# Optimization experiments

Hardware: AMD Instinct MI355X
Metric: run time of the kernel (lower is better)

The kernel has to match this reference:

```python
import jax, jax.numpy as jnp
import numpy as np
from math import sqrt

D_MODEL = 1024
HEADS = 16
D_K = D_MODEL // HEADS
NEG = -1e9


def setup_inputs() -> dict:
    key = jax.random.key(0)
    ks = jax.random.split(key, 8)
    bs, s, d = 2, 2048, D_MODEL
    inp = {
        "k": jax.random.normal(ks[0], (bs, s, d), jnp.float32),
        "v": jax.random.normal(ks[1], (bs, s, d), jnp.float32),
        "q": jax.random.normal(ks[2], (bs, s, d), jnp.float32),
        "mask": jax.random.randint(ks[3], (bs, s, 1), 0, 2).astype(jnp.int64),
        # torch nn.Linear weights: y = x @ W.T, W is [out, in]
        "Wq": jax.random.normal(ks[4], (d, d), jnp.float32) / sqrt(d),
        "Wk": jax.random.normal(ks[5], (d, d), jnp.float32) / sqrt(d),
        "Wv": jax.random.normal(ks[6], (d, d), jnp.float32) / sqrt(d),
        "Wo": jax.random.normal(ks[7], (d, d), jnp.float32) / sqrt(d),
    }
    return inp


def reference(k, v, q, mask, Wq, Wk, Wv, Wo):
    bs, s_k, d = k.shape
    s_q = q.shape[1]
    h, d_k = HEADS, D_K
    # linear projections (no bias), then split heads -> [bs, h, s, d_k]
    kh = (k @ Wk.T).reshape(bs, s_k, h, d_k).transpose(0, 2, 1, 3)
    vh = (v @ Wv.T).reshape(bs, s_k, h, d_k).transpose(0, 2, 1, 3)
    qh = (q @ Wq.T).reshape(bs, s_q, h, d_k).transpose(0, 2, 1, 3)
    # scaled dot-product scores [bs, h, s_q, s_k]
    scores = jnp.einsum("bhqd,bhkd->bhqk", qh, kh) / sqrt(d_k)
    # mask [bs, s_k, 1] -> [bs, 1, 1, s_k], masked positions get -1e9
    m = mask[:, None].transpose(0, 1, 3, 2)  # [bs,1,1,s_k]
    scores = jnp.where(m == 0, NEG, scores)
    probs = jax.nn.softmax(scores, axis=-1)  # dropout is identity (eval)
    attn = jnp.einsum("bhqk,bhkd->bhqd", probs, vh)
    attn_concat = attn.transpose(0, 2, 1, 3).reshape(bs, s_q, d)
    return attn_concat @ Wo.T
```

## Files before the change

### kernel.cpp

```cpp
#include <hip/hip_runtime.h>

typedef __bf16 bf16x8 __attribute__((ext_vector_type(8)));
typedef float f32x4 __attribute__((ext_vector_type(4)));

#define BS 2
#define SEQ 2048
#define DM 1024
#define NH 16
#define DKH 64
#define GM 4096
#define GN 1024
#define GK 1024
#define NEGV (-1e9f)

#define OFF_XQ 0u
#define OFF_XK 4194304u
#define OFF_XV 8388608u
#define OFF_WQ 12582912u
#define OFF_WK 13631488u
#define OFF_WV 14680064u
#define OFF_WO 15728640u
#define OFF_QH 16777216u
#define OFF_KC 20971520u
#define OFF_VT 25165824u
#define OFF_AT OFF_XQ

#if __has_builtin(__builtin_amdgcn_exp2f)
#define EXP2(x) __builtin_amdgcn_exp2f(x)
#else
static __device__ __forceinline__ float EXP2(float x) {
    float r;
    asm volatile("v_exp_f32 %0, %1" : "=v"(r) : "v"(x));
    return r;
}
#endif

__device__ __forceinline__ unsigned cvt_pk(float lo, float hi) {
    unsigned r;
    asm volatile("v_cvt_pk_bf16_f32 %0, %1, %2" : "=v"(r) : "v"(lo), "v"(hi));
    return r;
}

__device__ __forceinline__ unsigned short f2b(float f) {
    unsigned u = __builtin_bit_cast(unsigned, f);
    u += 0x7fffu + ((u >> 16) & 1u);
    return (unsigned short)(u >> 16);
}

typedef const __attribute__((address_space(1))) unsigned int* gas_t;
typedef __attribute__((address_space(3))) unsigned int* las_t;

__device__ __forceinline__ void gload_lds16(const ushort* g, ushort* l) {
    __builtin_amdgcn_global_load_lds((gas_t)(const void*)g, (las_t)(void*)l, 16, 0, 0);
}

#define BARRIER() __builtin_amdgcn_s_barrier()
#define VMCNT(n) asm volatile("s_waitcnt vmcnt(" #n ")" ::: "memory")

__global__ __launch_bounds__(256)
void cvt_kernel(const float* __restrict__ q, const float* __restrict__ k,
                const float* __restrict__ v, const float* __restrict__ wq,
                const float* __restrict__ wk, const float* __restrict__ wv,
                const float* __restrict__ wo, ushort* __restrict__ ws)
{
    const float* src; unsigned n; unsigned dst;
    switch (blockIdx.y) {
        case 0: src = q;  n = 4194304u; dst = OFF_XQ; break;
        case 1: src = k;  n = 4194304u; dst = OFF_XK; break;
        case 2: src = v;  n = 4194304u; dst = OFF_XV; break;
        case 3: src = wq; n = 1048576u; dst = OFF_WQ; break;
        case 4: src = wk; n = 1048576u; dst = OFF_WK; break;
        case 5: src = wv; n = 1048576u; dst = OFF_WV; break;
        default: src = wo; n = 1048576u; dst = OFF_WO; break;
    }
    unsigned i = (blockIdx.x * 256u + threadIdx.x) * 4u;
    if (i >= n) return;
    float4 f = *(const float4*)(src + i);
    ushort4 o;
    o.x = f2b(f.x); o.y = f2b(f.y); o.z = f2b(f.z); o.w = f2b(f.w);
    *(ushort4*)(ws + dst + i) = o;
}

__global__ __launch_bounds__(256)
void scan_kernel(const int* __restrict__ mask, int* __restrict__ cpos, int* __restrict__ mbuf)
{
    const int b = blockIdx.x;
    const int* mp = mask + (size_t)b * SEQ;
    const int tid = threadIdx.x;
    const int lane = tid & 63, w = tid >> 6;
    int v[8];
    int cnt = 0;
#pragma unroll
    for (int j = 0; j < 8; ++j) { v[j] = mp[tid * 8 + j]; cnt += (v[j] != 0); }
    int inc = cnt;
#pragma unroll
    for (int d = 1; d < 64; d <<= 1) {
        int t = __shfl_up(inc, d);
        if (lane >= d) inc += t;
    }
    __shared__ int wsum[4];
    if (lane == 63) wsum[w] = inc;
    __syncthreads();
    int base = inc - cnt;
    for (int i = 0; i < w; ++i) base += wsum[i];
    int c = base;
    int* ob = cpos + (size_t)b * SEQ;
#pragma unroll
    for (int j = 0; j < 8; ++j) {
        ob[tid * 8 + j] = (v[j] != 0) ? c : -1;
        c += (v[j] != 0);
    }
    if (tid == 255) mbuf[b] = base + cnt;
}

__global__ __launch_bounds__(512)
void gemm256(const ushort* __restrict__ Abase, const ushort* __restrict__ Bbase,
             ushort* __restrict__ wsbase, const int* __restrict__ cpos)
{
    __shared__ __align__(16) ushort lA[2][2][8192];
    __shared__ __align__(16) ushort lB[2][2][8192];

    const unsigned z = blockIdx.z;
    const ushort* A  = Abase + (size_t)z * (GM * GK);
    const ushort* Bw = Bbase + (size_t)z * (GN * GK);
    const float scale = (z == 0) ? 0.125f * 1.44269504088896f : 1.0f;

    const int tid = threadIdx.x;
    const int lane = tid & 63, wid = tid >> 6;
    const int wr = wid >> 2, wc = wid & 3;
    const int lr = lane & 15, lg = lane >> 4;
    const int srow8 = lane >> 3, scol = lane & 7;

    const int lin = blockIdx.y * 4 + blockIdx.x;
    const int xcd = lin & 7, kidx = lin >> 3;
    const int m0 = (xcd * 2 + (kidx >> 2)) * 256;
    const int n0 = (kidx & 3) * 256;

    f32x4 acc[8][4] = {};
    bf16x8 aq[4][2], aq2[4][2], b01[2][2], b23[2][2];

#define STAGE_A(s, h, t)                                                          \
    _Pragma("unroll") for (int c = 0; c < 2; ++c) {                               \
        int rih = (wid * 2 + c) * 8 + srow8;                                      \
        gload_lds16(A + (size_t)(m0 + (h) * 128 + rih) * GK + (t) * 64 +          \
                        ((scol ^ (rih & 7)) * 8),                                 \
                    &lA[s][h][(wid * 2 + c) * 512]);                              \
    }
#define STAGE_B(s, h, t)                                                          \
    _Pragma("unroll") for (int c = 0; c < 2; ++c) {                               \
        int rih = (wid * 2 + c) * 8 + srow8;                                      \
        gload_lds16(Bw + (size_t)(n0 + (h) * 128 + rih) * GK + (t) * 64 +         \
                         ((scol ^ (rih & 7)) * 8),                                \
                    &lB[s][h][(wid * 2 + c) * 512]);                              \
    }
#define LDA_FRAG(dst, s, ibase)                                                   \
    _Pragma("unroll") for (int i2 = 0; i2 < 4; ++i2)                              \
    _Pragma("unroll") for (int kk = 0; kk < 2; ++kk) {                            \
        int row = ((ibase) + i2) * 16 + lr;                                       \
        dst[i2][kk] = *(const bf16x8*)&lA[s][wr][row * 64 +                       \
                          (((kk * 4 + lg) ^ (row & 7)) * 8)];                     \
    }
#define LDB_FRAG(dst, s, jbase)                                                   \
    _Pragma("unroll") for (int j2 = 0; j2 < 2; ++j2)                              \
    _Pragma("unroll") for (int kk = 0; kk < 2; ++kk) {                            \
        int row = (wc & 1) * 64 + ((jbase) + j2) * 16 + lr;                       \
        dst[j2][kk] = *(const bf16x8*)&lB[s][wc >> 1][row * 64 +                  \
                          (((kk * 4 + lg) ^ (row & 7)) * 8)];                     \
    }
#define MMA_Q(ibase, jbase, av, bv)                                               \
    __builtin_amdgcn_s_setprio(1);                                                \
    _Pragma("unroll") for (int i2 = 0; i2 < 4; ++i2)                              \
    _Pragma("unroll") for (int j2 = 0; j2 < 2; ++j2)                              \
    _Pragma("unroll") for (int kk = 0; kk < 2; ++kk)                              \
        acc[(ibase) + i2][(jbase) + j2] = __builtin_amdgcn_mfma_f32_16x16x32_bf16(\
            av[i2][kk], bv[j2][kk], acc[(ibase) + i2][(jbase) + j2], 0, 0, 0);    \
    __builtin_amdgcn_s_setprio(0);

    STAGE_B(0, 0, 0); STAGE_B(0, 1, 0); STAGE_A(0, 0, 0); STAGE_A(0, 1, 0);
    STAGE_B(1, 0, 1); STAGE_B(1, 1, 1); STAGE_A(1, 0, 1); STAGE_A(1, 1, 1);
    VMCNT(8);
    BARRIER();

    for (int it = 0; it < 7; ++it) {
        const int t2 = 2 * it + 2, t3 = 2 * it + 3;
        LDA_FRAG(aq, 0, 0); LDB_FRAG(b01, 0, 0);
        BARRIER(); MMA_Q(0, 0, aq, b01); BARRIER();
        LDB_FRAG(b23, 0, 2);
        BARRIER(); MMA_Q(0, 2, aq, b23); BARRIER();
        LDA_FRAG(aq2, 0, 4);
        STAGE_B(0, 0, t2); STAGE_B(0, 1, t2);
        BARRIER(); MMA_Q(4, 2, aq2, b23); BARRIER();
        STAGE_A(0, 0, t2);
        VMCNT(6);
        BARRIER(); MMA_Q(4, 0, aq2, b01); BARRIER();
        LDA_FRAG(aq, 1, 0); LDB_FRAG(b01, 1, 0);
        STAGE_A(0, 1, t2);
        BARRIER(); MMA_Q(0, 0, aq, b01); BARRIER();
        LDB_FRAG(b23, 1, 2);
        BARRIER(); MMA_Q(0, 2, aq, b23); BARRIER();
        LDA_FRAG(aq2, 1, 4);
        STAGE_B(1, 0, t3); STAGE_B(1, 1, t3);
        BARRIER(); MMA_Q(4, 2, aq2, b23); BARRIER();
        STAGE_A(1, 0, t3); STAGE_A(1, 1, t3);
        VMCNT(8);
        BARRIER(); MMA_Q(4, 0, aq2, b01); BARRIER();
    }

    LDA_FRAG(aq, 0, 0); LDB_FRAG(b01, 0, 0);
    BARRIER(); MMA_Q(0, 0, aq, b01); BARRIER();
    LDB_FRAG(b23, 0, 2);
    BARRIER(); MMA_Q(0, 2, aq, b23); BARRIER();
    LDA_FRAG(aq2, 0, 4);
    BARRIER(); MMA_Q(4, 2, aq2, b23); BARRIER();
    VMCNT(0);
    BARRIER(); MMA_Q(4, 0, aq2, b01); BARRIER();
    LDA_FRAG(aq, 1, 0); LDB_FRAG(b01, 1, 0);
    BARRIER(); MMA_Q(0, 0, aq, b01); BARRIER();
    LDB_FRAG(b23, 1, 2);
    BARRIER(); MMA_Q(0, 2, aq, b23); BARRIER();
    LDA_FRAG(aq2, 1, 4);
    BARRIER(); MMA_Q(4, 2, aq2, b23); BARRIER();
    BARRIER(); MMA_Q(4, 0, aq2, b01); BARRIER();

    ushort* qh  = wsbase + OFF_QH;
    ushort* kc  = wsbase + OFF_KC;
    ushort* vtp = wsbase + OFF_VT;
#pragma unroll
    for (int i = 0; i < 8; ++i) {
#pragma unroll
        for (int r = 0; r < 4; ++r) {
            int row = m0 + wr * 128 + i * 16 + lg * 4 + r;
            int b = row >> 11, s = row & 2047;
            if (z == 0) {
#pragma unroll
                for (int j = 0; j < 4; ++j) {
                    int col = n0 + wc * 64 + j * 16 + lr;
                    qh[(((size_t)b * NH + (col >> 6)) * SEQ + s) * DKH + (col & 63)] =
                        f2b(acc[i][j][r] * scale);
                }
            } else {
                int c = cpos[b * SEQ + s];
                if (c >= 0) {
                    if (z == 1) {
#pragma unroll
                        for (int j = 0; j < 4; ++j) {
                            int col = n0 + wc * 64 + j * 16 + lr;
                            kc[(((size_t)b * NH + (col >> 6)) * SEQ + c) * DKH + (col & 63)] =
                                f2b(acc[i][j][r]);
                        }
                    } else {
                        int vt = (c & ~63) | ((c & 15) * 4 + ((c >> 4) & 3));
#pragma unroll
                        for (int j = 0; j < 4; ++j) {
                            int col = n0 + wc * 64 + j * 16 + lr;
                            vtp[(((size_t)b * NH + (col >> 6)) * DKH + (col & 63)) * SEQ + vt] =
                                f2b(acc[i][j][r]);
                        }
                    }
                }
            }
        }
    }
#undef STAGE_A
#undef STAGE_B
#undef LDA_FRAG
#undef LDB_FRAG
#undef MMA_Q
}

__global__ __launch_bounds__(256)
void gemm_bt(const ushort* __restrict__ A, const ushort* __restrict__ Bw,
             float* __restrict__ of)
{
    __shared__ __align__(16) ushort lA[128 * 64];
    __shared__ __align__(16) ushort lB[128 * 64];

    const int tid = threadIdx.x;
    const int lane = tid & 63, wid = tid >> 6;
    const int wr = wid >> 1, wc = wid & 1;
    const int lr = lane & 15, lg = lane >> 4;
    const int lin = blockIdx.y * 8 + blockIdx.x;
    const int swz = (lin & 7) * 32 + (lin >> 3);
    const int m0 = (swz >> 3) * 128, n0 = (swz & 7) * 128;
    const int srow = wid * 32 + (lane >> 3);
    const int scol = (lane & 7) * 8;

    f32x4 acc[4][4] = {};

    for (int k0 = 0; k0 < GK; k0 += 64) {
        __syncthreads();
#pragma unroll
        for (int p = 0; p < 4; ++p) {
            gload_lds16(A + (size_t)(m0 + srow + p * 8) * GK + k0 + scol,
                        &lA[(wid * 32 + p * 8) * 64]);
            gload_lds16(Bw + (size_t)(n0 + srow + p * 8) * GK + k0 + scol,
                        &lB[(wid * 32 + p * 8) * 64]);
        }
        __syncthreads();
#pragma unroll
        for (int kk = 0; kk < 2; ++kk) {
            bf16x8 af[4], bfr[4];
#pragma unroll
            for (int i = 0; i < 4; ++i) {
                af[i]  = *(const bf16x8*)(&lA[(wr * 64 + i * 16 + lr) * 64 + kk * 32 + lg * 8]);
                bfr[i] = *(const bf16x8*)(&lB[(wc * 64 + i * 16 + lr) * 64 + kk * 32 + lg * 8]);
            }
#pragma unroll
            for (int i = 0; i < 4; ++i)
#pragma unroll
                for (int j = 0; j < 4; ++j)
                    acc[i][j] = __builtin_amdgcn_mfma_f32_16x16x32_bf16(af[i], bfr[j], acc[i][j], 0, 0, 0);
        }
    }

#pragma unroll
    for (int i = 0; i < 4; ++i)
#pragma unroll
        for (int j = 0; j < 4; ++j) {
            int col = n0 + wc * 64 + j * 16 + lr;
#pragma unroll
            for (int r = 0; r < 4; ++r) {
                int row = m0 + wr * 64 + i * 16 + lg * 4 + r;
                of[(size_t)row * GN + col] = acc[i][j][r];
            }
        }
}

__global__ __launch_bounds__(256)
void attn_kernel(ushort* __restrict__ ws, const int* __restrict__ mbuf)
{
    const int bid = blockIdx.x;
    const int qt = bid & 31;
    const int h  = (bid >> 5) & 15;
    const int b  = bid >> 9;
    const int bh = b * NH + h;

    const ushort* Qp = ws + OFF_QH + (size_t)bh * (SEQ * DKH);
    const ushort* Kc = ws + OFF_KC + (size_t)bh * (SEQ * DKH);
    const ushort* VT = ws + OFF_VT + (size_t)bh * (DKH * SEQ);
    ushort* At = ws + OFF_AT;

    const int mb = mbuf[b];
    const int nt = (mb + 63) >> 6;

    __shared__ __align__(16) ushort lK[2][64 * 64];
    __shared__ __align__(16) ushort lV[2][64 * 64];
    __shared__ __align__(16) ushort lP[4][16][72];

    const int tid = threadIdx.x;
    const int lane = tid & 63, wid = tid >> 6;
    const int lr = lane & 15, lg = lane >> 4;
    ushort* lPw = &lP[wid][0][0];

    const int srow = wid * 16 + (lane >> 3);
    const int sg = lane & 7;

    const int qrow0 = qt * 64 + wid * 16;
    bf16x8 qf[2];
#pragma unroll
    for (int kk = 0; kk < 2; ++kk)
        qf[kk] = *(const bf16x8*)(Qp + (size_t)(qrow0 + lr) * DKH + kk * 32 + lg * 8);

    f32x4 acc_o[4] = {};
    float lrun[4] = {0.f, 0.f, 0.f, 0.f};

    auto STAGE = [&](int buf, int kt) {
        const int kbase = kt * 64;
#pragma unroll
        for (int c = 0; c < 2; ++c) {
            int r = srow + c * 8;
            gload_lds16(Kc + (size_t)(kbase + r) * DKH + ((sg ^ (r & 7)) * 8),
                        &lK[buf][(wid * 16 + c * 8) * 64]);
            gload_lds16(VT + (size_t)r * SEQ + kbase + ((sg ^ (r & 7)) * 8),
                        &lV[buf][(wid * 16 + c * 8) * 64]);
        }
    };

    STAGE(0, 0);
    __syncthreads();

    for (int kt = 0; kt < nt; ++kt) {
        const int cur = kt & 1;
        if (kt + 1 < nt) STAGE(cur ^ 1, kt + 1);
        const ushort* lKc = lK[cur];
        const ushort* lVc = lV[cur];

        f32x4 s[4];
        __builtin_amdgcn_s_setprio(1);
#pragma unroll
        for (int fc = 0; fc < 4; ++fc) {
            int row = fc * 16 + lr;
            int sw = row & 7;
            bf16x8 kf0 = *(const bf16x8*)(lKc + row * 64 + ((lg ^ sw) * 8));
            bf16x8 kf1 = *(const bf16x8*)(lKc + row * 64 + (((4 + lg) ^ sw) * 8));
            f32x4 t = {};
            t = __builtin_amdgcn_mfma_f32_16x16x32_bf16(qf[0], kf0, t, 0, 0, 0);
            t = __builtin_amdgcn_mfma_f32_16x16x32_bf16(qf[1], kf1, t, 0, 0, 0);
            s[fc] = t;
        }
        __builtin_amdgcn_s_setprio(0);

        if (kt == nt - 1) {
            const int kbase = kt * 64;
#pragma unroll
            for (int fc = 0; fc < 4; ++fc)
                if (kbase + fc * 16 + lr >= mb)
                    s[fc] = f32x4{NEGV, NEGV, NEGV, NEGV};
        }

#pragma unroll
        for (int r = 0; r < 4; ++r) {
            float p0 = EXP2(s[0][r]), p1 = EXP2(s[1][r]);
            float p2 = EXP2(s[2][r]), p3 = EXP2(s[3][r]);
            lrun[r] += (p0 + p1) + (p2 + p3);
            uint2 pk;
            pk.x = cvt_pk(p0, p1);
            pk.y = cvt_pk(p2, p3);
            *(uint2*)(lPw + (lg * 4 + r) * 72 + lr * 4) = pk;
        }

        __builtin_amdgcn_s_setprio(1);
#pragma unroll
        for (int kk = 0; kk < 2; ++kk) {
            bf16x8 pf = *(const bf16x8*)(lPw + lr * 72 + kk * 32 + lg * 8);
#pragma unroll
            for (int fc2 = 0; fc2 < 4; ++fc2) {
                int d = fc2 * 16 + lr;
                bf16x8 vf = *(const bf16x8*)(lVc + d * 64 + (((kk * 4 + lg) ^ (d & 7)) * 8));
                acc_o[fc2] = __builtin_amdgcn_mfma_f32_16x16x32_bf16(pf, vf, acc_o[fc2], 0, 0, 0);
            }
        }
        __builtin_amdgcn_s_setprio(0);
        __syncthreads();
    }

#pragma unroll
    for (int r = 0; r < 4; ++r) {
        float l = lrun[r];
        l += __shfl_xor(l, 1);
        l += __shfl_xor(l, 2);
        l += __shfl_xor(l, 4);
        l += __shfl_xor(l, 8);
        float rl = 1.0f / l;
        int qrow = qrow0 + lg * 4 + r;
#pragma unroll
        for (int fc2 = 0; fc2 < 4; ++fc2)
            At[((size_t)(b * SEQ) + qrow) * DM + h * DKH + fc2 * 16 + lr] =
                f2b(acc_o[fc2][r] * rl);
    }
}

extern "C" void kernel_launch(void* const* d_in, const int* in_sizes, int n_in,
                              void* d_out, int out_size, void* d_ws, size_t ws_size,
                              hipStream_t stream) {
    const float* kin = (const float*)d_in[0];
    const float* vin = (const float*)d_in[1];
    const float* qin = (const float*)d_in[2];
    const int*   msk = (const int*)d_in[3];
    const float* wq  = (const float*)d_in[4];
    const float* wk  = (const float*)d_in[5];
    const float* wv  = (const float*)d_in[6];
    const float* wo  = (const float*)d_in[7];
    ushort* ws = (ushort*)d_ws;
    float* out = (float*)d_out;
    int* cposb = (int*)d_out;
    int* mbuf = cposb + BS * SEQ;

    scan_kernel<<<2, 256, 0, stream>>>(msk, cposb, mbuf);
    cvt_kernel<<<dim3(4096, 7), 256, 0, stream>>>(qin, kin, vin, wq, wk, wv, wo, ws);
    gemm256<<<dim3(4, 16, 3), 512, 0, stream>>>(ws + OFF_XQ, ws + OFF_WQ, ws, cposb);
    attn_kernel<<<1024, 256, 0, stream>>>(ws, mbuf);
    gemm_bt<<<dim3(8, 32), 256, 0, stream>>>(ws + OFF_AT, ws + OFF_WO, out);
}
```

Before: 138.3 us.

## Process 128 query rows per attention block with two fragments per wave

Each attention workgroup now handles 128 query rows instead of 64, with every wave computing two 16-row query fragments against the same staged K and V tiles. K and V fragments read from LDS are reused across both fragments, which halves the global and LDS traffic for K/V per query row and halves the grid to 512 blocks. The trade-offs are higher register pressure, fewer blocks to fill the CUs, and a larger per-wave P buffer in LDS.

```diff
diff --git a/kernel.cpp b/kernel.cpp
--- a/kernel.cpp
+++ b/kernel.cpp
@@ -330,9 +330,9 @@
 void attn_kernel(ushort* __restrict__ ws, const int* __restrict__ mbuf)
 {
     const int bid = blockIdx.x;
-    const int qt = bid & 31;
-    const int h  = (bid >> 5) & 15;
-    const int b  = bid >> 9;
+    const int qt = bid & 15;
+    const int h  = (bid >> 4) & 15;
+    const int b  = bid >> 8;
     const int bh = b * NH + h;
 
     const ushort* Qp = ws + OFF_QH + (size_t)bh * (SEQ * DKH);
@@ -345,7 +345,7 @@
 
     __shared__ __align__(16) ushort lK[2][64 * 64];
     __shared__ __align__(16) ushort lV[2][64 * 64];
-    __shared__ __align__(16) ushort lP[4][16][72];
+    __shared__ __align__(16) ushort lP[4][32][72];
 
     const int tid = threadIdx.x;
     const int lane = tid & 63, wid = tid >> 6;
@@ -355,14 +355,16 @@
     const int srow = wid * 16 + (lane >> 3);
     const int sg = lane & 7;
 
-    const int qrow0 = qt * 64 + wid * 16;
-    bf16x8 qf[2];
-#pragma unroll
-    for (int kk = 0; kk < 2; ++kk)
-        qf[kk] = *(const bf16x8*)(Qp + (size_t)(qrow0 + lr) * DKH + kk * 32 + lg * 8);
-
-    f32x4 acc_o[4] = {};
-    float lrun[4] = {0.f, 0.f, 0.f, 0.f};
+    const int qrow0 = qt * 128 + wid * 32;
+    bf16x8 qf[2][2];
+#pragma unroll
+    for (int fr = 0; fr < 2; ++fr)
+#pragma unroll
+        for (int kk = 0; kk < 2; ++kk)
+            qf[fr][kk] = *(const bf16x8*)(Qp + (size_t)(qrow0 + fr * 16 + lr) * DKH + kk * 32 + lg * 8);
+
+    f32x4 acc_o[2][4] = {};
+    float lrun[2][4] = {};
 
     auto STAGE = [&](int buf, int kt) {
         const int kbase = kt * 64;
@@ -385,7 +387,7 @@
         const ushort* lKc = lK[cur];
         const ushort* lVc = lV[cur];
 
-        f32x4 s[4];
+        f32x4 s[2][4];
         __builtin_amdgcn_s_setprio(1);
 #pragma unroll
         for (int fc = 0; fc < 4; ++fc) {
@@ -393,10 +395,13 @@
             int sw = row & 7;
             bf16x8 kf0 = *(const bf16x8*)(lKc + row * 64 + ((lg ^ sw) * 8));
             bf16x8 kf1 = *(const bf16x8*)(lKc + row * 64 + (((4 + lg) ^ sw) * 8));
-            f32x4 t = {};
-            t = __builtin_amdgcn_mfma_f32_16x16x32_bf16(qf[0], kf0, t, 0, 0, 0);
-            t = __builtin_amdgcn_mfma_f32_16x16x32_bf16(qf[1], kf1, t, 0, 0, 0);
-            s[fc] = t;
+#pragma unroll
+            for (int fr = 0; fr < 2; ++fr) {
+                f32x4 t = {};
+                t = __builtin_amdgcn_mfma_f32_16x16x32_bf16(qf[fr][0], kf0, t, 0, 0, 0);
+                t = __builtin_amdgcn_mfma_f32_16x16x32_bf16(qf[fr][1], kf1, t, 0, 0, 0);
+                s[fr][fc] = t;
+            }
         }
         __builtin_amdgcn_s_setprio(0);
 
@@ -405,29 +410,38 @@
 #pragma unroll
             for (int fc = 0; fc < 4; ++fc)
                 if (kbase + fc * 16 + lr >= mb)
-                    s[fc] = f32x4{NEGV, NEGV, NEGV, NEGV};
-        }
-
-#pragma unroll
-        for (int r = 0; r < 4; ++r) {
-            float p0 = EXP2(s[0][r]), p1 = EXP2(s[1][r]);
-            float p2 = EXP2(s[2][r]), p3 = EXP2(s[3][r]);
-            lrun[r] += (p0 + p1) + (p2 + p3);
-            uint2 pk;
-            pk.x = cvt_pk(p0, p1);
-            pk.y = cvt_pk(p2, p3);
-            *(uint2*)(lPw + (lg * 4 + r) * 72 + lr * 4) = pk;
-        }
+#pragma unroll
+                    for (int fr = 0; fr < 2; ++fr)
+                        s[fr][fc] = f32x4{NEGV, NEGV, NEGV, NEGV};
+        }
+
+#pragma unroll
+        for (int fr = 0; fr < 2; ++fr)
+#pragma unroll
+            for (int r = 0; r < 4; ++r) {
+                float p0 = EXP2(s[fr][0][r]), p1 = EXP2(s[fr][1][r]);
+                float p2 = EXP2(s[fr][2][r]), p3 = EXP2(s[fr][3][r]);
+                lrun[fr][r] += (p0 + p1) + (p2 + p3);
+                uint2 pk;
+                pk.x = cvt_pk(p0, p1);
+                pk.y = cvt_pk(p2, p3);
+                *(uint2*)(lPw + (fr * 16 + lg * 4 + r) * 72 + lr * 4) = pk;
+            }
 
         __builtin_amdgcn_s_setprio(1);
 #pragma unroll
         for (int kk = 0; kk < 2; ++kk) {
-            bf16x8 pf = *(const bf16x8*)(lPw + lr * 72 + kk * 32 + lg * 8);
+            bf16x8 pf[2];
+#pragma unroll
+            for (int fr = 0; fr < 2; ++fr)
+                pf[fr] = *(const bf16x8*)(lPw + (fr * 16 + lr) * 72 + kk * 32 + lg * 8);
 #pragma unroll
             for (int fc2 = 0; fc2 < 4; ++fc2) {
                 int d = fc2 * 16 + lr;
                 bf16x8 vf = *(const bf16x8*)(lVc + d * 64 + (((kk * 4 + lg) ^ (d & 7)) * 8));
-                acc_o[fc2] = __builtin_amdgcn_mfma_f32_16x16x32_bf16(pf, vf, acc_o[fc2], 0, 0, 0);
+#pragma unroll
+                for (int fr = 0; fr < 2; ++fr)
+                    acc_o[fr][fc2] = __builtin_amdgcn_mfma_f32_16x16x32_bf16(pf[fr], vf, acc_o[fr][fc2], 0, 0, 0);
             }
         }
         __builtin_amdgcn_s_setprio(0);
@@ -435,19 +449,21 @@
     }
 
 #pragma unroll
-    for (int r = 0; r < 4; ++r) {
-        float l = lrun[r];
-        l += __shfl_xor(l, 1);
-        l += __shfl_xor(l, 2);
-        l += __shfl_xor(l, 4);
-        l += __shfl_xor(l, 8);
-        float rl = 1.0f / l;
-        int qrow = qrow0 + lg * 4 + r;
-#pragma unroll
-        for (int fc2 = 0; fc2 < 4; ++fc2)
-            At[((size_t)(b * SEQ) + qrow) * DM + h * DKH + fc2 * 16 + lr] =
-                f2b(acc_o[fc2][r] * rl);
-    }
+    for (int fr = 0; fr < 2; ++fr)
+#pragma unroll
+        for (int r = 0; r < 4; ++r) {
+            float l = lrun[fr][r];
+            l += __shfl_xor(l, 1);
+            l += __shfl_xor(l, 2);
+            l += __shfl_xor(l, 4);
+            l += __shfl_xor(l, 8);
+            float rl = 1.0f / l;
+            int qrow = qrow0 + fr * 16 + lg * 4 + r;
+#pragma unroll
+            for (int fc2 = 0; fc2 < 4; ++fc2)
+                At[((size_t)(b * SEQ) + qrow) * DM + h * DKH + fc2 * 16 + lr] =
+                    f2b(acc_o[fr][fc2][r] * rl);
+        }
 }
 
 extern "C" void kernel_launch(void* const* d_in, const int* in_sizes, int n_in,
@@ -469,6 +485,6 @@
     scan_kernel<<<2, 256, 0, stream>>>(msk, cposb, mbuf);
     cvt_kernel<<<dim3(4096, 7), 256, 0, stream>>>(qin, kin, vin, wq, wk, wv, wo, ws);
     gemm256<<<dim3(4, 16, 3), 512, 0, stream>>>(ws + OFF_XQ, ws + OFF_WQ, ws, cposb);
-    attn_kernel<<<1024, 256, 0, stream>>>(ws, mbuf);
+    attn_kernel<<<512, 256, 0, stream>>>(ws, mbuf);
     gemm_bt<<<dim3(8, 32), 256, 0, stream>>>(ws + OFF_AT, ws + OFF_WO, out);
 }
```

Result: faster. 128.6 us (-7.0%).
